# Kernel optimization log

Hardware: AMD Instinct MI355X
Metric: run time of the kernel (lower is better)

Reference implementation:

```python
import jax, jax.numpy as jnp
import numpy as np

N_NODES = 100000
N_EDGES = 1000000

def _gcn_conv(x, W, b, src, dst, n_nodes):
    # PyG GCNConv: linear first, then symmetric-normalized aggregation with self loops
    x = x @ W  # [N, F_out]
    loop = jnp.arange(n_nodes, dtype=src.dtype)
    src2 = jnp.concatenate([src, loop])
    dst2 = jnp.concatenate([dst, loop])
    deg = jax.ops.segment_sum(jnp.ones(src2.shape[0], x.dtype), dst2, num_segments=n_nodes)
    dinv = jnp.where(deg > 0, jax.lax.rsqrt(deg), 0.0)
    norm = dinv[src2] * dinv[dst2]  # [E+N]
    msgs = x[src2] * norm[:, None]  # gather + scale
    out = jax.ops.segment_sum(msgs, dst2, num_segments=n_nodes)  # scatter-add
    return out + b

def _pair_norm_si(x):
    # mode 'PN-SI', scale=1
    x = x - x.mean(axis=0)
    row_norm = jnp.sqrt(1e-6 + jnp.sum(x * x, axis=1, keepdims=True))
    return x / row_norm

def setup_inputs() -> dict:
    key = jax.random.key(0)
    k1, k2, k3, k4 = jax.random.split(key, 4)
    in_c, hid_c, out_c = 256, 64, 40
    x = jax.random.normal(k1, (N_NODES, in_c), dtype=jnp.float32)
    edge_index = jax.random.randint(k2, (2, N_EDGES), 0, N_NODES, dtype=jnp.int64)
    W1 = jax.random.normal(k3, (in_c, hid_c), dtype=jnp.float32) / np.sqrt(in_c)
    b1 = jnp.zeros((hid_c,), jnp.float32)
    W2 = jax.random.normal(k4, (hid_c, out_c), dtype=jnp.float32) / np.sqrt(hid_c)
    b2 = jnp.zeros((out_c,), jnp.float32)
    return {"x": x, "edge_index": edge_index, "W1": W1, "b1": b1, "W2": W2, "b2": b2}

def reference(x, edge_index, W1, b1, W2, b2):
    src, dst = edge_index[0], edge_index[1]
    n = x.shape[0]
    h = jax.nn.relu(_gcn_conv(x, W1, b1, src, dst, n))
    h = _gcn_conv(h, W2, b2, src, dst, n)
    h = _pair_norm_si(h)
    return jax.nn.log_softmax(h, axis=1)
```

## Files before the change

### kernel.cpp

```cpp
#include <hip/hip_runtime.h>
#include <hip/hip_fp16.h>
#include <math.h>

#define F_IN  256
#define F_HID 64
#define F_OUT 40
#define HS2_LD 64

typedef _Float16 h8 __attribute__((ext_vector_type(8)));
typedef _Float16 h4 __attribute__((ext_vector_type(4)));
typedef float f4 __attribute__((ext_vector_type(4)));

__global__ void k_deg(const int* __restrict__ dst, unsigned* __restrict__ degc, int E) {
    int i = blockIdx.x * blockDim.x + threadIdx.x;
    if (i < E) atomicAdd(&degc[dst[i]], 1u);
}

__global__ __launch_bounds__(256) void k_scanA(const unsigned* __restrict__ degc,
                                               unsigned* __restrict__ exscan,
                                               unsigned* __restrict__ bsum, int N) {
    __shared__ unsigned s[256];
    int tid = threadIdx.x;
    int i = blockIdx.x * 256 + tid;
    unsigned v = (i < N) ? ((degc[i] + 8u) & ~7u) : 0u;
    s[tid] = v;
    __syncthreads();
    for (int off = 1; off < 256; off <<= 1) {
        unsigned t = (tid >= off) ? s[tid - off] : 0u;
        __syncthreads();
        s[tid] += t;
        __syncthreads();
    }
    if (i < N) exscan[i] = s[tid] - v;
    if (tid == 255) bsum[blockIdx.x] = s[255];
}

__global__ __launch_bounds__(512) void k_scanB(unsigned* __restrict__ bsum, int nb) {
    __shared__ unsigned s[512];
    int tid = threadIdx.x;
    unsigned v = (tid < nb) ? bsum[tid] : 0u;
    s[tid] = v;
    __syncthreads();
    for (int off = 1; off < 512; off <<= 1) {
        unsigned t = (tid >= off) ? s[tid - off] : 0u;
        __syncthreads();
        s[tid] += t;
        __syncthreads();
    }
    if (tid < nb) bsum[tid] = s[tid] - v;
}

__global__ void k_scanC(const unsigned* __restrict__ degc, const unsigned* __restrict__ exscan,
                        const unsigned* __restrict__ bsum, unsigned* __restrict__ rowptr,
                        float* __restrict__ dinv, int N) {
    int i = blockIdx.x * blockDim.x + threadIdx.x;
    if (i < N) {
        unsigned rp = exscan[i] + bsum[i >> 8];
        rowptr[i] = rp;
        dinv[i] = rsqrtf((float)degc[i] + 1.0f);
        if (i == N - 1) rowptr[N] = rp + ((degc[i] + 8u) & ~7u);
        if (i == 0) dinv[N] = 1.0f;
    }
}

__global__ void k_fill(const int* __restrict__ src, const int* __restrict__ dst,
                       const unsigned* __restrict__ rowptr, unsigned* __restrict__ cursor,
                       unsigned* __restrict__ colp, int E) {
    int e = blockIdx.x * blockDim.x + threadIdx.x;
    if (e >= E) return;
    int d = dst[e];
    unsigned p = atomicAdd(&cursor[d], 1u);
    colp[rowptr[d] + p] = (unsigned)src[e];
}

__global__ void k_pad(const unsigned* __restrict__ degc, const unsigned* __restrict__ rowptr,
                      unsigned* __restrict__ colp, int N) {
    int i = blockIdx.x * blockDim.x + threadIdx.x;
    if (i >= N) return;
    unsigned d = degc[i];
    unsigned base = rowptr[i];
    unsigned pd = (d + 8u) & ~7u;
    colp[base + d] = (unsigned)i;
    for (unsigned p = d + 1; p < pd; ++p) colp[base + p] = (unsigned)N;
}

__global__ void k_wt(const float* __restrict__ W1, __half* __restrict__ Wt) {
    int i = blockIdx.x * 256 + threadIdx.x;
    int k = i >> 6, n = i & 63;
    Wt[n * 256 + k] = __float2half(W1[i]);
}

__global__ void k_w2t(const float* __restrict__ W2, __half* __restrict__ W2t) {
    int i = blockIdx.x * 256 + threadIdx.x;
    int n = i >> 6, k = i & 63;
    W2t[n * 64 + k] = __float2half((n < F_OUT) ? W2[k * F_OUT + n] : 0.f);
}

#define XS 136
__global__ __launch_bounds__(256) void k_mm1(const float* __restrict__ x,
                                             const __half* __restrict__ Wth,
                                             const float* __restrict__ dinv,
                                             __half* __restrict__ hs1o, int N) {
    __shared__ _Float16 sX[64 * XS];
    const _Float16* Wt = (const _Float16*)Wth;
    _Float16* hs1 = (_Float16*)hs1o;
    int tid = threadIdx.x;
    int lane = tid & 63;
    int wv = tid >> 6;
    int m15 = lane & 15;
    int q = lane >> 4;
    int nbase = blockIdx.x * 64;

    h8 bf[8];
    #pragma unroll
    for (int kt = 0; kt < 8; ++kt)
        bf[kt] = *(const h8*)(Wt + (wv * 16 + m15) * 256 + kt * 32 + q * 8);

    f4 acc[4];
    #pragma unroll
    for (int mt = 0; mt < 4; ++mt) acc[mt] = (f4){0.f, 0.f, 0.f, 0.f};

    #pragma unroll
    for (int c = 0; c < 2; ++c) {
        #pragma unroll
        for (int p = 0; p < 8; ++p) {
            int idx = p * 256 + tid;
            int row = idx >> 5;
            int c4  = idx & 31;
            int node = nbase + row;
            float4 v = (node < N) ? *(const float4*)(x + (size_t)node * F_IN + c * 128 + c4 * 4)
                                  : make_float4(0.f, 0.f, 0.f, 0.f);
            h4 hv = { (_Float16)v.x, (_Float16)v.y, (_Float16)v.z, (_Float16)v.w };
            *(h4*)&sX[row * XS + c4 * 4] = hv;
        }
        __syncthreads();
        #pragma unroll
        for (int kt2 = 0; kt2 < 4; ++kt2) {
            #pragma unroll
            for (int mt = 0; mt < 4; ++mt) {
                h8 a = *(const h8*)&sX[(mt * 16 + m15) * XS + kt2 * 32 + q * 8];
                acc[mt] = __builtin_amdgcn_mfma_f32_16x16x32_f16(a, bf[c * 4 + kt2], acc[mt], 0, 0, 0);
            }
        }
        __syncthreads();
    }

    #pragma unroll
    for (int mt = 0; mt < 4; ++mt) {
        #pragma unroll
        for (int r = 0; r < 4; ++r) {
            int node = nbase + mt * 16 + q * 4 + r;
            if (node <= N) {
                float din = (node < N) ? dinv[node] : 1.0f;
                hs1[(size_t)node * F_HID + wv * 16 + m15] = (_Float16)(acc[mt][r] * din);
            }
        }
    }
}

__global__ __launch_bounds__(256) void k_agg1(const unsigned* __restrict__ rowptr,
                                              const unsigned* __restrict__ colp,
                                              const float* __restrict__ dinv,
                                              const __half* __restrict__ hs1o,
                                              const float* __restrict__ bias1,
                                              __half* __restrict__ agg1o, int N) {
    const _Float16* hp = (const _Float16*)hs1o;
    _Float16* agg1h = (_Float16*)agg1o;
    int lane = threadIdx.x & 63;
    int w = blockIdx.x * 4 + (threadIdx.x >> 6);
    int na = 2 * w, nb = 2 * w + 1;
    if (na >= N) return;
    int g = lane >> 3, c = lane & 7;

    float accA[8], accB[8];
    #pragma unroll
    for (int j = 0; j < 8; ++j) { accA[j] = 0.f; accB[j] = 0.f; }

    unsigned aE = rowptr[na], aEnd = rowptr[na + 1];
    bool hasB = (nb < N);
    unsigned bE = 0, bEnd = 0;
    if (hasB) { bE = rowptr[nb]; bEnd = rowptr[nb + 1]; }

    while (aE < aEnd && bE < bEnd) {
        unsigned sA = colp[aE + g];
        unsigned sB = colp[bE + g];
        h8 va = *(const h8*)(hp + (size_t)sA * F_HID + c * 8);
        h8 vb = *(const h8*)(hp + (size_t)sB * F_HID + c * 8);
        #pragma unroll
        for (int j = 0; j < 8; ++j) { accA[j] += (float)va[j]; accB[j] += (float)vb[j]; }
        aE += 8; bE += 8;
    }
    while (aE < aEnd) {
        unsigned sA = colp[aE + g];
        h8 va = *(const h8*)(hp + (size_t)sA * F_HID + c * 8);
        #pragma unroll
        for (int j = 0; j < 8; ++j) accA[j] += (float)va[j];
        aE += 8;
    }
    while (bE < bEnd) {
        unsigned sB = colp[bE + g];
        h8 vb = *(const h8*)(hp + (size_t)sB * F_HID + c * 8);
        #pragma unroll
        for (int j = 0; j < 8; ++j) accB[j] += (float)vb[j];
        bE += 8;
    }

    #pragma unroll
    for (int off = 8; off <= 32; off <<= 1) {
        #pragma unroll
        for (int j = 0; j < 8; ++j) {
            accA[j] += __shfl_xor(accA[j], off, 64);
            accB[j] += __shfl_xor(accB[j], off, 64);
        }
    }

    if (g == 0) {
        float bv[8];
        *(float4*)&bv[0] = *(const float4*)(bias1 + c * 8);
        *(float4*)&bv[4] = *(const float4*)(bias1 + c * 8 + 4);
        float dinA = dinv[na];
        h8 ho;
        #pragma unroll
        for (int j = 0; j < 8; ++j) ho[j] = (_Float16)fmaxf(accA[j] * dinA + bv[j], 0.f);
        *(h8*)(agg1h + (size_t)na * F_HID + c * 8) = ho;
        if (hasB) {
            float dinB = dinv[nb];
            #pragma unroll
            for (int j = 0; j < 8; ++j) ho[j] = (_Float16)fmaxf(accB[j] * dinB + bv[j], 0.f);
            *(h8*)(agg1h + (size_t)nb * F_HID + c * 8) = ho;
        }
    }
}

#define AS 72
__global__ __launch_bounds__(256) void k_mm2(const __half* __restrict__ agg1o,
                                             const __half* __restrict__ W2th,
                                             const float* __restrict__ dinv,
                                             __half* __restrict__ hs2o, int N) {
    __shared__ _Float16 sA[64 * AS];
    const _Float16* agg1h = (const _Float16*)agg1o;
    const _Float16* W2t = (const _Float16*)W2th;
    _Float16* hs2 = (_Float16*)hs2o;
    int tid = threadIdx.x;
    int lane = tid & 63;
    int wv = tid >> 6;
    int m15 = lane & 15;
    int q = lane >> 4;
    int nbase = blockIdx.x * 64;

    h8 bf[2];
    #pragma unroll
    for (int kt = 0; kt < 2; ++kt)
        bf[kt] = *(const h8*)(W2t + (wv * 16 + m15) * 64 + kt * 32 + q * 8);

    #pragma unroll
    for (int p = 0; p < 2; ++p) {
        int idx = p * 256 + tid;
        int row = idx >> 3;
        int c8  = idx & 7;
        int node = nbase + row;
        h8 v;
        if (node < N) v = *(const h8*)(agg1h + (size_t)node * F_HID + c8 * 8);
        else          v = (h8){0, 0, 0, 0, 0, 0, 0, 0};
        *(h8*)&sA[row * AS + c8 * 8] = v;
    }
    __syncthreads();

    f4 acc[4];
    #pragma unroll
    for (int mt = 0; mt < 4; ++mt) acc[mt] = (f4){0.f, 0.f, 0.f, 0.f};
    #pragma unroll
    for (int kt = 0; kt < 2; ++kt) {
        #pragma unroll
        for (int mt = 0; mt < 4; ++mt) {
            h8 a = *(const h8*)&sA[(mt * 16 + m15) * AS + kt * 32 + q * 8];
            acc[mt] = __builtin_amdgcn_mfma_f32_16x16x32_f16(a, bf[kt], acc[mt], 0, 0, 0);
        }
    }

    #pragma unroll
    for (int mt = 0; mt < 4; ++mt) {
        #pragma unroll
        for (int r = 0; r < 4; ++r) {
            int node = nbase + mt * 16 + q * 4 + r;
            if (node <= N) {
                float din = (node < N) ? dinv[node] : 1.0f;
                hs2[(size_t)node * HS2_LD + wv * 16 + m15] = (_Float16)(acc[mt][r] * din);
            }
        }
    }
}

__global__ __launch_bounds__(256) void k_agg2(const unsigned* __restrict__ rowptr,
                                              const unsigned* __restrict__ colp,
                                              const float* __restrict__ dinv,
                                              const __half* __restrict__ hs2o,
                                              float* __restrict__ out,
                                              float* __restrict__ colsum, int N) {
    __shared__ float part[4][8][8];
    const _Float16* hp = (const _Float16*)hs2o;
    int lane = threadIdx.x & 63;
    int wv = threadIdx.x >> 6;
    int g = lane >> 3, c = lane & 7;
    int nwaves = gridDim.x * 4;
    float csum[8];
    #pragma unroll
    for (int j = 0; j < 8; ++j) csum[j] = 0.f;

    for (int w = blockIdx.x * 4 + wv; 2 * w < N; w += nwaves) {
        int na = 2 * w, nb = 2 * w + 1;
        float accA[8], accB[8];
        #pragma unroll
        for (int j = 0; j < 8; ++j) { accA[j] = 0.f; accB[j] = 0.f; }

        unsigned aE = rowptr[na], aEnd = rowptr[na + 1];
        bool hasB = (nb < N);
        unsigned bE = 0, bEnd = 0;
        if (hasB) { bE = rowptr[nb]; bEnd = rowptr[nb + 1]; }

        while (aE < aEnd && bE < bEnd) {
            unsigned sA = colp[aE + g];
            unsigned sB = colp[bE + g];
            h8 va = *(const h8*)(hp + (size_t)sA * HS2_LD + c * 8);
            h8 vb = *(const h8*)(hp + (size_t)sB * HS2_LD + c * 8);
            #pragma unroll
            for (int j = 0; j < 8; ++j) { accA[j] += (float)va[j]; accB[j] += (float)vb[j]; }
            aE += 8; bE += 8;
        }
        while (aE < aEnd) {
            unsigned sA = colp[aE + g];
            h8 va = *(const h8*)(hp + (size_t)sA * HS2_LD + c * 8);
            #pragma unroll
            for (int j = 0; j < 8; ++j) accA[j] += (float)va[j];
            aE += 8;
        }
        while (bE < bEnd) {
            unsigned sB = colp[bE + g];
            h8 vb = *(const h8*)(hp + (size_t)sB * HS2_LD + c * 8);
            #pragma unroll
            for (int j = 0; j < 8; ++j) accB[j] += (float)vb[j];
            bE += 8;
        }

        #pragma unroll
        for (int off = 8; off <= 32; off <<= 1) {
            #pragma unroll
            for (int j = 0; j < 8; ++j) {
                accA[j] += __shfl_xor(accA[j], off, 64);
                accB[j] += __shfl_xor(accB[j], off, 64);
            }
        }

        if (g == 0) {
            float dinA = dinv[na];
            #pragma unroll
            for (int j = 0; j < 8; ++j) { accA[j] *= dinA; csum[j] += accA[j]; }
            if (c < 5) {
                *(float4*)(out + (size_t)na * F_OUT + c * 8) =
                    make_float4(accA[0], accA[1], accA[2], accA[3]);
                *(float4*)(out + (size_t)na * F_OUT + c * 8 + 4) =
                    make_float4(accA[4], accA[5], accA[6], accA[7]);
            }
            if (hasB) {
                float dinB = dinv[nb];
                #pragma unroll
                for (int j = 0; j < 8; ++j) { accB[j] *= dinB; csum[j] += accB[j]; }
                if (c < 5) {
                    *(float4*)(out + (size_t)nb * F_OUT + c * 8) =
                        make_float4(accB[0], accB[1], accB[2], accB[3]);
                    *(float4*)(out + (size_t)nb * F_OUT + c * 8 + 4) =
                        make_float4(accB[4], accB[5], accB[6], accB[7]);
                }
            }
        }
    }

    if (g == 0) {
        #pragma unroll
        for (int j = 0; j < 8; ++j) part[wv][c][j] = csum[j];
    }
    __syncthreads();
    int tid = threadIdx.x;
    if (tid < F_OUT) {
        int cc = tid >> 3, jj = tid & 7;
        float s = part[0][cc][jj] + part[1][cc][jj] + part[2][cc][jj] + part[3][cc][jj];
        atomicAdd(&colsum[tid], s);
    }
}

__global__ __launch_bounds__(128) void k_final(float* __restrict__ out,
                                               const float* __restrict__ colsum, int N) {
    __shared__ float sMean[F_OUT];
    if (threadIdx.x < F_OUT) sMean[threadIdx.x] = colsum[threadIdx.x] * (1.0f / (float)N);
    __syncthreads();
    int n = blockIdx.x * blockDim.x + threadIdx.x;
    if (n >= N) return;
    float* row = out + (size_t)n * F_OUT;
    float v[F_OUT];
    float ss = 0.f;
    #pragma unroll
    for (int f = 0; f < F_OUT; ++f) {
        float t = row[f] - sMean[f];
        v[f] = t;
        ss += t * t;
    }
    float scale = 1.0f / sqrtf(ss + 1e-6f);
    float m = -1e30f;
    #pragma unroll
    for (int f = 0; f < F_OUT; ++f) {
        float y = v[f] * scale;
        v[f] = y;
        m = fmaxf(m, y);
    }
    float sum = 0.f;
    #pragma unroll
    for (int f = 0; f < F_OUT; ++f) sum += expf(v[f] - m);
    float lse = logf(sum);
    #pragma unroll
    for (int f = 0; f < F_OUT; ++f) row[f] = v[f] - m - lse;
}

extern "C" void kernel_launch(void* const* d_in, const int* in_sizes, int n_in,
                              void* d_out, int out_size, void* d_ws, size_t ws_size,
                              hipStream_t stream) {
    const float* x  = (const float*)d_in[0];
    const int*   ei = (const int*)d_in[1];
    const float* W1 = (const float*)d_in[2];
    const float* b1 = (const float*)d_in[3];
    const float* W2 = (const float*)d_in[4];
    float* out = (float*)d_out;

    int N = in_sizes[0] / F_IN;
    int E = in_sizes[1] / 2;
    const int* src = ei;
    const int* dst = ei + E;

    char* p = (char*)d_ws;
    auto alloc = [&](size_t bytes) { char* r = p; p += (bytes + 127) & ~(size_t)127; return r; };
    unsigned* degc   = (unsigned*)alloc((size_t)N * 4);
    unsigned* cursor = (unsigned*)alloc((size_t)N * 4);
    float*    colsum = (float*)   alloc(64 * 4);
    unsigned* rowptr = (unsigned*)alloc((size_t)(N + 1) * 4);
    unsigned* colp   = (unsigned*)alloc((size_t)(E + 8 * N + 8) * 4);
    float*    dinv   = (float*)   alloc((size_t)(N + 1) * 4);
    __half*   agg1h  = (__half*)  alloc((size_t)64 * (N + 1) * 2);
    __half*   hs1    = (__half*)  alloc((size_t)64 * (N + 1) * 2);
    __half*   hs2    = (__half*)  alloc((size_t)64 * (N + 1) * 2);
    __half*   Wt     = (__half*)  alloc((size_t)16384 * 2);
    __half*   W2t    = (__half*)  alloc((size_t)4096 * 2);
    unsigned* exscan = (unsigned*)agg1h;
    unsigned* bsum   = exscan + N;

    hipMemsetAsync(d_ws, 0, (char*)(colsum + 64) - (char*)d_ws, stream);

    int nA = (N + 255) / 256;
    k_deg<<<(E + 255) / 256, 256, 0, stream>>>(dst, degc, E);
    k_scanA<<<nA, 256, 0, stream>>>(degc, exscan, bsum, N);
    k_scanB<<<1, 512, 0, stream>>>(bsum, nA);
    k_scanC<<<nA, 256, 0, stream>>>(degc, exscan, bsum, rowptr, dinv, N);
    k_fill<<<(E + 255) / 256, 256, 0, stream>>>(src, dst, rowptr, cursor, colp, E);
    k_pad<<<nA, 256, 0, stream>>>(degc, rowptr, colp, N);
    k_wt<<<64, 256, 0, stream>>>(W1, Wt);
    k_w2t<<<16, 256, 0, stream>>>(W2, W2t);
    k_mm1<<<(N + 63) / 64, 256, 0, stream>>>(x, Wt, dinv, hs1, N);
    int waves1 = (N + 1) / 2;
    k_agg1<<<(waves1 + 3) / 4, 256, 0, stream>>>(rowptr, colp, dinv, hs1, b1, agg1h, N);
    k_mm2<<<(N + 64) / 64, 256, 0, stream>>>(agg1h, W2t, dinv, hs2, N);
    k_agg2<<<2048, 256, 0, stream>>>(rowptr, colp, dinv, hs2, out, colsum, N);
    k_final<<<(N + 127) / 128, 128, 0, stream>>>(out, colsum, N);
}
```

Measured before the change: 404.8 us.

## Store layer-2 features in FP8 and merge fill/pad and weight-prep launches

Layer-2 pre-aggregation features are written as FP8 e4m3 bytes instead of fp16, which halves the bytes gathered per edge in the second aggregation kernel. The fill and pad kernels are merged into one launch, and the two weight-transpose kernels become a single launch, cutting launch overhead. The FP8 storage lowers precision of the intermediate features and adds per-element decode work in the gather loop, which may affect accuracy tolerance.

```diff
diff --git a/kernel.cpp b/kernel.cpp
--- a/kernel.cpp
+++ b/kernel.cpp
@@ -1,15 +1,20 @@
 #include <hip/hip_runtime.h>
 #include <hip/hip_fp16.h>
+#include <hip/hip_fp8.h>
 #include <math.h>
 
 #define F_IN  256
 #define F_HID 64
 #define F_OUT 40
-#define HS2_LD 64
+#define HS2B  64
 
 typedef _Float16 h8 __attribute__((ext_vector_type(8)));
 typedef _Float16 h4 __attribute__((ext_vector_type(4)));
 typedef float f4 __attribute__((ext_vector_type(4)));
+
+__device__ inline float f8tof(unsigned b) {
+    __hip_fp8_e4m3 t; t.__x = (__hip_fp8_storage_t)b; return (float)t;
+}
 
 __global__ void k_deg(const int* __restrict__ dst, unsigned* __restrict__ degc, int E) {
     int i = blockIdx.x * blockDim.x + threadIdx.x;
@@ -63,37 +68,36 @@
     }
 }
 
-__global__ void k_fill(const int* __restrict__ src, const int* __restrict__ dst,
-                       const unsigned* __restrict__ rowptr, unsigned* __restrict__ cursor,
-                       unsigned* __restrict__ colp, int E) {
-    int e = blockIdx.x * blockDim.x + threadIdx.x;
-    if (e >= E) return;
-    int d = dst[e];
-    unsigned p = atomicAdd(&cursor[d], 1u);
-    colp[rowptr[d] + p] = (unsigned)src[e];
-}
-
-__global__ void k_pad(const unsigned* __restrict__ degc, const unsigned* __restrict__ rowptr,
-                      unsigned* __restrict__ colp, int N) {
-    int i = blockIdx.x * blockDim.x + threadIdx.x;
-    if (i >= N) return;
-    unsigned d = degc[i];
-    unsigned base = rowptr[i];
-    unsigned pd = (d + 8u) & ~7u;
-    colp[base + d] = (unsigned)i;
-    for (unsigned p = d + 1; p < pd; ++p) colp[base + p] = (unsigned)N;
-}
-
-__global__ void k_wt(const float* __restrict__ W1, __half* __restrict__ Wt) {
+__global__ void k_fillpad(const int* __restrict__ src, const int* __restrict__ dst,
+                          const unsigned* __restrict__ degc,
+                          const unsigned* __restrict__ rowptr, unsigned* __restrict__ cursor,
+                          unsigned* __restrict__ colp, int E, int N) {
+    int t = blockIdx.x * blockDim.x + threadIdx.x;
+    if (t < E) {
+        int d = dst[t];
+        unsigned p = atomicAdd(&cursor[d], 1u);
+        colp[rowptr[d] + p] = (unsigned)src[t];
+    } else if (t < E + N) {
+        int i = t - E;
+        unsigned d = degc[i];
+        unsigned base = rowptr[i];
+        unsigned pd = (d + 8u) & ~7u;
+        colp[base + d] = (unsigned)i;
+        for (unsigned p = d + 1; p < pd; ++p) colp[base + p] = (unsigned)N;
+    }
+}
+
+__global__ void k_wprep(const float* __restrict__ W1, const float* __restrict__ W2,
+                        __half* __restrict__ Wt, __half* __restrict__ W2t) {
     int i = blockIdx.x * 256 + threadIdx.x;
-    int k = i >> 6, n = i & 63;
-    Wt[n * 256 + k] = __float2half(W1[i]);
-}
-
-__global__ void k_w2t(const float* __restrict__ W2, __half* __restrict__ W2t) {
-    int i = blockIdx.x * 256 + threadIdx.x;
-    int n = i >> 6, k = i & 63;
-    W2t[n * 64 + k] = __float2half((n < F_OUT) ? W2[k * F_OUT + n] : 0.f);
+    if (i < 16384) {
+        int k = i >> 6, n = i & 63;
+        Wt[n * 256 + k] = __float2half(W1[i]);
+    } else if (i < 20480) {
+        int j = i - 16384;
+        int n = j >> 6, k = j & 63;
+        W2t[n * 64 + k] = __float2half((n < F_OUT) ? W2[k * F_OUT + n] : 0.f);
+    }
 }
 
 #define XS 136
@@ -236,11 +240,10 @@
 __global__ __launch_bounds__(256) void k_mm2(const __half* __restrict__ agg1o,
                                              const __half* __restrict__ W2th,
                                              const float* __restrict__ dinv,
-                                             __half* __restrict__ hs2o, int N) {
+                                             unsigned char* __restrict__ hs2b, int N) {
     __shared__ _Float16 sA[64 * AS];
     const _Float16* agg1h = (const _Float16*)agg1o;
     const _Float16* W2t = (const _Float16*)W2th;
-    _Float16* hs2 = (_Float16*)hs2o;
     int tid = threadIdx.x;
     int lane = tid & 63;
     int wv = tid >> 6;
@@ -285,7 +288,8 @@
             int node = nbase + mt * 16 + q * 4 + r;
             if (node <= N) {
                 float din = (node < N) ? dinv[node] : 1.0f;
-                hs2[(size_t)node * HS2_LD + wv * 16 + m15] = (_Float16)(acc[mt][r] * din);
+                __hip_fp8_e4m3 f8((float)(acc[mt][r] * din));
+                hs2b[(size_t)node * HS2B + wv * 16 + m15] = (unsigned char)f8.__x;
             }
         }
     }
@@ -294,11 +298,10 @@
 __global__ __launch_bounds__(256) void k_agg2(const unsigned* __restrict__ rowptr,
                                               const unsigned* __restrict__ colp,
                                               const float* __restrict__ dinv,
-                                              const __half* __restrict__ hs2o,
+                                              const unsigned char* __restrict__ hs2b,
                                               float* __restrict__ out,
                                               float* __restrict__ colsum, int N) {
     __shared__ float part[4][8][8];
-    const _Float16* hp = (const _Float16*)hs2o;
     int lane = threadIdx.x & 63;
     int wv = threadIdx.x >> 6;
     int g = lane >> 3, c = lane & 7;
@@ -321,24 +324,35 @@
         while (aE < aEnd && bE < bEnd) {
             unsigned sA = colp[aE + g];
             unsigned sB = colp[bE + g];
-            h8 va = *(const h8*)(hp + (size_t)sA * HS2_LD + c * 8);
-            h8 vb = *(const h8*)(hp + (size_t)sB * HS2_LD + c * 8);
-            #pragma unroll
-            for (int j = 0; j < 8; ++j) { accA[j] += (float)va[j]; accB[j] += (float)vb[j]; }
+            uint2 va = *(const uint2*)(hs2b + (size_t)sA * HS2B + c * 8);
+            uint2 vb = *(const uint2*)(hs2b + (size_t)sB * HS2B + c * 8);
+            #pragma unroll
+            for (int j = 0; j < 4; ++j) {
+                accA[j]     += f8tof((va.x >> (8 * j)) & 0xFF);
+                accA[j + 4] += f8tof((va.y >> (8 * j)) & 0xFF);
+                accB[j]     += f8tof((vb.x >> (8 * j)) & 0xFF);
+                accB[j + 4] += f8tof((vb.y >> (8 * j)) & 0xFF);
+            }
             aE += 8; bE += 8;
         }
         while (aE < aEnd) {
             unsigned sA = colp[aE + g];
-            h8 va = *(const h8*)(hp + (size_t)sA * HS2_LD + c * 8);
-            #pragma unroll
-            for (int j = 0; j < 8; ++j) accA[j] += (float)va[j];
+            uint2 va = *(const uint2*)(hs2b + (size_t)sA * HS2B + c * 8);
+            #pragma unroll
+            for (int j = 0; j < 4; ++j) {
+                accA[j]     += f8tof((va.x >> (8 * j)) & 0xFF);
+                accA[j + 4] += f8tof((va.y >> (8 * j)) & 0xFF);
+            }
             aE += 8;
         }
         while (bE < bEnd) {
             unsigned sB = colp[bE + g];
-            h8 vb = *(const h8*)(hp + (size_t)sB * HS2_LD + c * 8);
-            #pragma unroll
-            for (int j = 0; j < 8; ++j) accB[j] += (float)vb[j];
+            uint2 vb = *(const uint2*)(hs2b + (size_t)sB * HS2B + c * 8);
+            #pragma unroll
+            for (int j = 0; j < 4; ++j) {
+                accB[j]     += f8tof((vb.x >> (8 * j)) & 0xFF);
+                accB[j + 4] += f8tof((vb.y >> (8 * j)) & 0xFF);
+            }
             bE += 8;
         }
 
@@ -445,7 +459,7 @@
     float*    dinv   = (float*)   alloc((size_t)(N + 1) * 4);
     __half*   agg1h  = (__half*)  alloc((size_t)64 * (N + 1) * 2);
     __half*   hs1    = (__half*)  alloc((size_t)64 * (N + 1) * 2);
-    __half*   hs2    = (__half*)  alloc((size_t)64 * (N + 1) * 2);
+    unsigned char* hs2b = (unsigned char*)alloc((size_t)HS2B * (N + 1));
     __half*   Wt     = (__half*)  alloc((size_t)16384 * 2);
     __half*   W2t    = (__half*)  alloc((size_t)4096 * 2);
     unsigned* exscan = (unsigned*)agg1h;
@@ -458,14 +472,12 @@
     k_scanA<<<nA, 256, 0, stream>>>(degc, exscan, bsum, N);
     k_scanB<<<1, 512, 0, stream>>>(bsum, nA);
     k_scanC<<<nA, 256, 0, stream>>>(degc, exscan, bsum, rowptr, dinv, N);
-    k_fill<<<(E + 255) / 256, 256, 0, stream>>>(src, dst, rowptr, cursor, colp, E);
-    k_pad<<<nA, 256, 0, stream>>>(degc, rowptr, colp, N);
-    k_wt<<<64, 256, 0, stream>>>(W1, Wt);
-    k_w2t<<<16, 256, 0, stream>>>(W2, W2t);
+    k_fillpad<<<(E + N + 255) / 256, 256, 0, stream>>>(src, dst, degc, rowptr, cursor, colp, E, N);
+    k_wprep<<<80, 256, 0, stream>>>(W1, W2, Wt, W2t);
     k_mm1<<<(N + 63) / 64, 256, 0, stream>>>(x, Wt, dinv, hs1, N);
     int waves1 = (N + 1) / 2;
     k_agg1<<<(waves1 + 3) / 4, 256, 0, stream>>>(rowptr, colp, dinv, hs1, b1, agg1h, N);
-    k_mm2<<<(N + 64) / 64, 256, 0, stream>>>(agg1h, W2t, dinv, hs2, N);
-    k_agg2<<<2048, 256, 0, stream>>>(rowptr, colp, dinv, hs2, out, colsum, N);
+    k_mm2<<<(N + 64) / 64, 256, 0, stream>>>(agg1h, W2t, dinv, hs2b, N);
+    k_agg2<<<2048, 256, 0, stream>>>(rowptr, colp, dinv, hs2b, out, colsum, N);
     k_final<<<(N + 127) / 128, 128, 0, stream>>>(out, colsum, N);
 }
```

Measured after the change: 406.4 us. No clear change (+0.4%).

## Fuse layer-1 aggregation into second matmul and merge small setup kernels

Applied to the files above, without the earlier changes.

Combines the first-layer gather/aggregation with the second-layer MFMA matmul, so the aggregated, ReLU'd features go straight into shared memory instead of a global agg1 buffer that gets written and read back. It also merges the CSR fill and pad kernels into one launch, and the two weight-transpose kernels into one. This cuts a global round trip of an N×64 half tensor and three kernel launches. In exchange, each block now runs 8 sequential node-pair aggregation passes per wave, which lowers parallelism per launch and may expose gather latency.

```diff
diff --git a/kernel.cpp b/kernel.cpp
--- a/kernel.cpp
+++ b/kernel.cpp
@@ -63,37 +63,36 @@
     }
 }
 
-__global__ void k_fill(const int* __restrict__ src, const int* __restrict__ dst,
-                       const unsigned* __restrict__ rowptr, unsigned* __restrict__ cursor,
-                       unsigned* __restrict__ colp, int E) {
-    int e = blockIdx.x * blockDim.x + threadIdx.x;
-    if (e >= E) return;
-    int d = dst[e];
-    unsigned p = atomicAdd(&cursor[d], 1u);
-    colp[rowptr[d] + p] = (unsigned)src[e];
-}
-
-__global__ void k_pad(const unsigned* __restrict__ degc, const unsigned* __restrict__ rowptr,
-                      unsigned* __restrict__ colp, int N) {
-    int i = blockIdx.x * blockDim.x + threadIdx.x;
-    if (i >= N) return;
-    unsigned d = degc[i];
-    unsigned base = rowptr[i];
-    unsigned pd = (d + 8u) & ~7u;
-    colp[base + d] = (unsigned)i;
-    for (unsigned p = d + 1; p < pd; ++p) colp[base + p] = (unsigned)N;
-}
-
-__global__ void k_wt(const float* __restrict__ W1, __half* __restrict__ Wt) {
+__global__ void k_fillpad(const int* __restrict__ src, const int* __restrict__ dst,
+                          const unsigned* __restrict__ degc,
+                          const unsigned* __restrict__ rowptr, unsigned* __restrict__ cursor,
+                          unsigned* __restrict__ colp, int E, int N) {
+    int t = blockIdx.x * blockDim.x + threadIdx.x;
+    if (t < E) {
+        int d = dst[t];
+        unsigned p = atomicAdd(&cursor[d], 1u);
+        colp[rowptr[d] + p] = (unsigned)src[t];
+    } else if (t < E + N) {
+        int i = t - E;
+        unsigned d = degc[i];
+        unsigned base = rowptr[i];
+        unsigned pd = (d + 8u) & ~7u;
+        colp[base + d] = (unsigned)i;
+        for (unsigned p = d + 1; p < pd; ++p) colp[base + p] = (unsigned)N;
+    }
+}
+
+__global__ void k_wprep(const float* __restrict__ W1, const float* __restrict__ W2,
+                        __half* __restrict__ Wt, __half* __restrict__ W2t) {
     int i = blockIdx.x * 256 + threadIdx.x;
-    int k = i >> 6, n = i & 63;
-    Wt[n * 256 + k] = __float2half(W1[i]);
-}
-
-__global__ void k_w2t(const float* __restrict__ W2, __half* __restrict__ W2t) {
-    int i = blockIdx.x * 256 + threadIdx.x;
-    int n = i >> 6, k = i & 63;
-    W2t[n * 64 + k] = __float2half((n < F_OUT) ? W2[k * F_OUT + n] : 0.f);
+    if (i < 16384) {
+        int k = i >> 6, n = i & 63;
+        Wt[n * 256 + k] = __float2half(W1[i]);
+    } else if (i < 20480) {
+        int j = i - 16384;
+        int n = j >> 6, k = j & 63;
+        W2t[n * 64 + k] = __float2half((n < F_OUT) ? W2[k * F_OUT + n] : 0.f);
+    }
 }
 
 #define XS 136
@@ -158,87 +157,16 @@
     }
 }
 
-__global__ __launch_bounds__(256) void k_agg1(const unsigned* __restrict__ rowptr,
-                                              const unsigned* __restrict__ colp,
-                                              const float* __restrict__ dinv,
-                                              const __half* __restrict__ hs1o,
-                                              const float* __restrict__ bias1,
-                                              __half* __restrict__ agg1o, int N) {
+#define AS 72
+__global__ __launch_bounds__(256) void k_aggmm2(const unsigned* __restrict__ rowptr,
+                                                const unsigned* __restrict__ colp,
+                                                const float* __restrict__ dinv,
+                                                const __half* __restrict__ hs1o,
+                                                const float* __restrict__ bias1,
+                                                const __half* __restrict__ W2th,
+                                                __half* __restrict__ hs2o, int N) {
+    __shared__ _Float16 sA[64 * AS];
     const _Float16* hp = (const _Float16*)hs1o;
-    _Float16* agg1h = (_Float16*)agg1o;
-    int lane = threadIdx.x & 63;
-    int w = blockIdx.x * 4 + (threadIdx.x >> 6);
-    int na = 2 * w, nb = 2 * w + 1;
-    if (na >= N) return;
-    int g = lane >> 3, c = lane & 7;
-
-    float accA[8], accB[8];
-    #pragma unroll
-    for (int j = 0; j < 8; ++j) { accA[j] = 0.f; accB[j] = 0.f; }
-
-    unsigned aE = rowptr[na], aEnd = rowptr[na + 1];
-    bool hasB = (nb < N);
-    unsigned bE = 0, bEnd = 0;
-    if (hasB) { bE = rowptr[nb]; bEnd = rowptr[nb + 1]; }
-
-    while (aE < aEnd && bE < bEnd) {
-        unsigned sA = colp[aE + g];
-        unsigned sB = colp[bE + g];
-        h8 va = *(const h8*)(hp + (size_t)sA * F_HID + c * 8);
-        h8 vb = *(const h8*)(hp + (size_t)sB * F_HID + c * 8);
-        #pragma unroll
-        for (int j = 0; j < 8; ++j) { accA[j] += (float)va[j]; accB[j] += (float)vb[j]; }
-        aE += 8; bE += 8;
-    }
-    while (aE < aEnd) {
-        unsigned sA = colp[aE + g];
-        h8 va = *(const h8*)(hp + (size_t)sA * F_HID + c * 8);
-        #pragma unroll
-        for (int j = 0; j < 8; ++j) accA[j] += (float)va[j];
-        aE += 8;
-    }
-    while (bE < bEnd) {
-        unsigned sB = colp[bE + g];
-        h8 vb = *(const h8*)(hp + (size_t)sB * F_HID + c * 8);
-        #pragma unroll
-        for (int j = 0; j < 8; ++j) accB[j] += (float)vb[j];
-        bE += 8;
-    }
-
-    #pragma unroll
-    for (int off = 8; off <= 32; off <<= 1) {
-        #pragma unroll
-        for (int j = 0; j < 8; ++j) {
-            accA[j] += __shfl_xor(accA[j], off, 64);
-            accB[j] += __shfl_xor(accB[j], off, 64);
-        }
-    }
-
-    if (g == 0) {
-        float bv[8];
-        *(float4*)&bv[0] = *(const float4*)(bias1 + c * 8);
-        *(float4*)&bv[4] = *(const float4*)(bias1 + c * 8 + 4);
-        float dinA = dinv[na];
-        h8 ho;
-        #pragma unroll
-        for (int j = 0; j < 8; ++j) ho[j] = (_Float16)fmaxf(accA[j] * dinA + bv[j], 0.f);
-        *(h8*)(agg1h + (size_t)na * F_HID + c * 8) = ho;
-        if (hasB) {
-            float dinB = dinv[nb];
-            #pragma unroll
-            for (int j = 0; j < 8; ++j) ho[j] = (_Float16)fmaxf(accB[j] * dinB + bv[j], 0.f);
-            *(h8*)(agg1h + (size_t)nb * F_HID + c * 8) = ho;
-        }
-    }
-}
-
-#define AS 72
-__global__ __launch_bounds__(256) void k_mm2(const __half* __restrict__ agg1o,
-                                             const __half* __restrict__ W2th,
-                                             const float* __restrict__ dinv,
-                                             __half* __restrict__ hs2o, int N) {
-    __shared__ _Float16 sA[64 * AS];
-    const _Float16* agg1h = (const _Float16*)agg1o;
     const _Float16* W2t = (const _Float16*)W2th;
     _Float16* hs2 = (_Float16*)hs2o;
     int tid = threadIdx.x;
@@ -246,23 +174,77 @@
     int wv = tid >> 6;
     int m15 = lane & 15;
     int q = lane >> 4;
+    int g = lane >> 3, c = lane & 7;
     int nbase = blockIdx.x * 64;
 
-    h8 bf[2];
+    h8 bfW[2];
     #pragma unroll
     for (int kt = 0; kt < 2; ++kt)
-        bf[kt] = *(const h8*)(W2t + (wv * 16 + m15) * 64 + kt * 32 + q * 8);
-
-    #pragma unroll
-    for (int p = 0; p < 2; ++p) {
-        int idx = p * 256 + tid;
-        int row = idx >> 3;
-        int c8  = idx & 7;
-        int node = nbase + row;
-        h8 v;
-        if (node < N) v = *(const h8*)(agg1h + (size_t)node * F_HID + c8 * 8);
-        else          v = (h8){0, 0, 0, 0, 0, 0, 0, 0};
-        *(h8*)&sA[row * AS + c8 * 8] = v;
+        bfW[kt] = *(const h8*)(W2t + (wv * 16 + m15) * 64 + kt * 32 + q * 8);
+
+    float bv[8];
+    *(float4*)&bv[0] = *(const float4*)(bias1 + c * 8);
+    *(float4*)&bv[4] = *(const float4*)(bias1 + c * 8 + 4);
+
+    for (int p2 = 0; p2 < 8; ++p2) {
+        int rowA = wv * 16 + 2 * p2;
+        int na = nbase + rowA, nb = na + 1;
+        bool doA = (na < N), doB = (nb < N);
+
+        float accA[8], accB[8];
+        #pragma unroll
+        for (int j = 0; j < 8; ++j) { accA[j] = 0.f; accB[j] = 0.f; }
+
+        unsigned aE = 0, aEnd = 0, bE = 0, bEnd = 0;
+        if (doA) { aE = rowptr[na]; aEnd = rowptr[na + 1]; }
+        if (doB) { bE = rowptr[nb]; bEnd = rowptr[nb + 1]; }
+
+        while (aE < aEnd && bE < bEnd) {
+            unsigned sAi = colp[aE + g];
+            unsigned sBi = colp[bE + g];
+            h8 va = *(const h8*)(hp + (size_t)sAi * F_HID + c * 8);
+            h8 vb = *(const h8*)(hp + (size_t)sBi * F_HID + c * 8);
+            #pragma unroll
+            for (int j = 0; j < 8; ++j) { accA[j] += (float)va[j]; accB[j] += (float)vb[j]; }
+            aE += 8; bE += 8;
+        }
+        while (aE < aEnd) {
+            unsigned sAi = colp[aE + g];
+            h8 va = *(const h8*)(hp + (size_t)sAi * F_HID + c * 8);
+            #pragma unroll
+            for (int j = 0; j < 8; ++j) accA[j] += (float)va[j];
+            aE += 8;
+        }
+        while (bE < bEnd) {
+            unsigned sBi = colp[bE + g];
+            h8 vb = *(const h8*)(hp + (size_t)sBi * F_HID + c * 8);
+            #pragma unroll
+            for (int j = 0; j < 8; ++j) accB[j] += (float)vb[j];
+            bE += 8;
+        }
+
+        #pragma unroll
+        for (int off = 8; off <= 32; off <<= 1) {
+            #pragma unroll
+            for (int j = 0; j < 8; ++j) {
+                accA[j] += __shfl_xor(accA[j], off, 64);
+                accB[j] += __shfl_xor(accB[j], off, 64);
+            }
+        }
+
+        if (g == 0) {
+            h8 ho;
+            float dinA = doA ? dinv[na] : 0.f;
+            #pragma unroll
+            for (int j = 0; j < 8; ++j)
+                ho[j] = doA ? (_Float16)fmaxf(accA[j] * dinA + bv[j], 0.f) : (_Float16)0.f;
+            *(h8*)&sA[rowA * AS + c * 8] = ho;
+            float dinB = doB ? dinv[nb] : 0.f;
+            #pragma unroll
+            for (int j = 0; j < 8; ++j)
+                ho[j] = doB ? (_Float16)fmaxf(accB[j] * dinB + bv[j], 0.f) : (_Float16)0.f;
+            *(h8*)&sA[(rowA + 1) * AS + c * 8] = ho;
+        }
     }
     __syncthreads();
 
@@ -274,7 +256,7 @@
         #pragma unroll
         for (int mt = 0; mt < 4; ++mt) {
             h8 a = *(const h8*)&sA[(mt * 16 + m15) * AS + kt * 32 + q * 8];
-            acc[mt] = __builtin_amdgcn_mfma_f32_16x16x32_f16(a, bf[kt], acc[mt], 0, 0, 0);
+            acc[mt] = __builtin_amdgcn_mfma_f32_16x16x32_f16(a, bfW[kt], acc[mt], 0, 0, 0);
         }
     }
 
@@ -443,12 +425,11 @@
     unsigned* rowptr = (unsigned*)alloc((size_t)(N + 1) * 4);
     unsigned* colp   = (unsigned*)alloc((size_t)(E + 8 * N + 8) * 4);
     float*    dinv   = (float*)   alloc((size_t)(N + 1) * 4);
-    __half*   agg1h  = (__half*)  alloc((size_t)64 * (N + 1) * 2);
     __half*   hs1    = (__half*)  alloc((size_t)64 * (N + 1) * 2);
     __half*   hs2    = (__half*)  alloc((size_t)64 * (N + 1) * 2);
     __half*   Wt     = (__half*)  alloc((size_t)16384 * 2);
     __half*   W2t    = (__half*)  alloc((size_t)4096 * 2);
-    unsigned* exscan = (unsigned*)agg1h;
+    unsigned* exscan = (unsigned*)hs2;
     unsigned* bsum   = exscan + N;
 
     hipMemsetAsync(d_ws, 0, (char*)(colsum + 64) - (char*)d_ws, stream);
@@ -458,14 +439,10 @@
     k_scanA<<<nA, 256, 0, stream>>>(degc, exscan, bsum, N);
     k_scanB<<<1, 512, 0, stream>>>(bsum, nA);
     k_scanC<<<nA, 256, 0, stream>>>(degc, exscan, bsum, rowptr, dinv, N);
-    k_fill<<<(E + 255) / 256, 256, 0, stream>>>(src, dst, rowptr, cursor, colp, E);
-    k_pad<<<nA, 256, 0, stream>>>(degc, rowptr, colp, N);
-    k_wt<<<64, 256, 0, stream>>>(W1, Wt);
-    k_w2t<<<16, 256, 0, stream>>>(W2, W2t);
+    k_fillpad<<<(E + N + 255) / 256, 256, 0, stream>>>(src, dst, degc, rowptr, cursor, colp, E, N);
+    k_wprep<<<80, 256, 0, stream>>>(W1, W2, Wt, W2t);
     k_mm1<<<(N + 63) / 64, 256, 0, stream>>>(x, Wt, dinv, hs1, N);
-    int waves1 = (N + 1) / 2;
-    k_agg1<<<(waves1 + 3) / 4, 256, 0, stream>>>(rowptr, colp, dinv, hs1, b1, agg1h, N);
-    k_mm2<<<(N + 64) / 64, 256, 0, stream>>>(agg1h, W2t, dinv, hs2, N);
+    k_aggmm2<<<(N + 64) / 64, 256, 0, stream>>>(rowptr, colp, dinv, hs1, b1, W2t, hs2, N);
     k_agg2<<<2048, 256, 0, stream>>>(rowptr, colp, dinv, hs2, out, colsum, N);
     k_final<<<(N + 127) / 128, 128, 0, stream>>>(out, colsum, N);
 }
```

Measured after the change: 416.0 us. +2.8%, slower.

## Fuse CSR-build preprocessing kernels and use single-pass decoupled-lookback scan

Applied to the files above, without the earlier changes.

Merges degree counting with the weight transposes, replaces the three-kernel scan with one decoupled-lookback scan that also zeroes cursor and colsum, and merges edge fill with row padding. This cuts the preprocessing from eight launches to three and shrinks the memset, reducing launch gaps and small-kernel tails. The lookback spins on flag words, so it depends on blocks taking tickets in order and on forward progress. Padding now uses eight threads per node.

```diff
diff --git a/kernel.cpp b/kernel.cpp
--- a/kernel.cpp
+++ b/kernel.cpp
@@ -11,18 +11,42 @@
 typedef _Float16 h4 __attribute__((ext_vector_type(4)));
 typedef float f4 __attribute__((ext_vector_type(4)));
 
-__global__ void k_deg(const int* __restrict__ dst, unsigned* __restrict__ degc, int E) {
-    int i = blockIdx.x * blockDim.x + threadIdx.x;
-    if (i < E) atomicAdd(&degc[dst[i]], 1u);
-}
-
-__global__ __launch_bounds__(256) void k_scanA(const unsigned* __restrict__ degc,
-                                               unsigned* __restrict__ exscan,
-                                               unsigned* __restrict__ bsum, int N) {
+__global__ void k_degw(const int* __restrict__ dst, unsigned* __restrict__ degc, int E,
+                       const float* __restrict__ W1, const float* __restrict__ W2,
+                       __half* __restrict__ Wt, __half* __restrict__ W2t) {
+    int i = blockIdx.x * 256 + threadIdx.x;
+    if (i < E) {
+        atomicAdd(&degc[dst[i]], 1u);
+        return;
+    }
+    int j = i - E;
+    if (j < 16384) {
+        int k = j >> 6, n = j & 63;
+        Wt[n * 256 + k] = __float2half(W1[j]);
+    } else if (j < 20480) {
+        int jj = j - 16384;
+        int n = jj >> 6, k = jj & 63;
+        W2t[n * 64 + k] = __float2half((n < F_OUT) ? W2[k * F_OUT + n] : 0.f);
+    }
+}
+
+__global__ __launch_bounds__(256) void k_scan(const unsigned* __restrict__ degc,
+                                              unsigned* __restrict__ aggf,
+                                              unsigned* __restrict__ ticket,
+                                              unsigned* __restrict__ rowptr,
+                                              float* __restrict__ dinv,
+                                              unsigned* __restrict__ cursor,
+                                              float* __restrict__ colsum, int N) {
     __shared__ unsigned s[256];
+    __shared__ unsigned sTick, sPfx, sTot;
     int tid = threadIdx.x;
-    int i = blockIdx.x * 256 + tid;
-    unsigned v = (i < N) ? ((degc[i] + 8u) & ~7u) : 0u;
+    if (tid == 0) sTick = atomicAdd(ticket, 1u);
+    if (blockIdx.x == 0 && tid < 64) colsum[tid] = 0.f;
+    __syncthreads();
+    unsigned b = sTick;
+    int i = (int)b * 256 + tid;
+    unsigned d = (i < N) ? degc[i] : 0u;
+    unsigned v = (i < N) ? ((d + 8u) & ~7u) : 0u;
     s[tid] = v;
     __syncthreads();
     for (int off = 1; off < 256; off <<= 1) {
@@ -31,69 +55,55 @@
         s[tid] += t;
         __syncthreads();
     }
-    if (i < N) exscan[i] = s[tid] - v;
-    if (tid == 255) bsum[blockIdx.x] = s[255];
-}
-
-__global__ __launch_bounds__(512) void k_scanB(unsigned* __restrict__ bsum, int nb) {
-    __shared__ unsigned s[512];
-    int tid = threadIdx.x;
-    unsigned v = (tid < nb) ? bsum[tid] : 0u;
-    s[tid] = v;
-    __syncthreads();
-    for (int off = 1; off < 512; off <<= 1) {
-        unsigned t = (tid >= off) ? s[tid - off] : 0u;
-        __syncthreads();
-        s[tid] += t;
-        __syncthreads();
-    }
-    if (tid < nb) bsum[tid] = s[tid] - v;
-}
-
-__global__ void k_scanC(const unsigned* __restrict__ degc, const unsigned* __restrict__ exscan,
-                        const unsigned* __restrict__ bsum, unsigned* __restrict__ rowptr,
-                        float* __restrict__ dinv, int N) {
-    int i = blockIdx.x * blockDim.x + threadIdx.x;
+    unsigned incl = s[tid];
+    if (tid == 255) {
+        sTot = s[255];
+        atomicExch(&aggf[b], s[255] | 0x40000000u);
+    }
+    __syncthreads();
+    if (tid == 0) {
+        unsigned run = 0;
+        int pr = (int)b - 1;
+        while (pr >= 0) {
+            unsigned t;
+            do { t = atomicAdd(&aggf[pr], 0u); } while ((t >> 30) == 0u);
+            run += t & 0x3FFFFFFFu;
+            if ((t >> 30) == 3u) break;
+            --pr;
+        }
+        sPfx = run;
+        atomicExch(&aggf[b], (run + sTot) | 0xC0000000u);
+    }
+    __syncthreads();
+    unsigned pfx = sPfx;
     if (i < N) {
-        unsigned rp = exscan[i] + bsum[i >> 8];
-        rowptr[i] = rp;
-        dinv[i] = rsqrtf((float)degc[i] + 1.0f);
-        if (i == N - 1) rowptr[N] = rp + ((degc[i] + 8u) & ~7u);
-        if (i == 0) dinv[N] = 1.0f;
-    }
-}
-
-__global__ void k_fill(const int* __restrict__ src, const int* __restrict__ dst,
-                       const unsigned* __restrict__ rowptr, unsigned* __restrict__ cursor,
-                       unsigned* __restrict__ colp, int E) {
-    int e = blockIdx.x * blockDim.x + threadIdx.x;
-    if (e >= E) return;
-    int d = dst[e];
-    unsigned p = atomicAdd(&cursor[d], 1u);
-    colp[rowptr[d] + p] = (unsigned)src[e];
-}
-
-__global__ void k_pad(const unsigned* __restrict__ degc, const unsigned* __restrict__ rowptr,
-                      unsigned* __restrict__ colp, int N) {
-    int i = blockIdx.x * blockDim.x + threadIdx.x;
-    if (i >= N) return;
-    unsigned d = degc[i];
-    unsigned base = rowptr[i];
-    unsigned pd = (d + 8u) & ~7u;
-    colp[base + d] = (unsigned)i;
-    for (unsigned p = d + 1; p < pd; ++p) colp[base + p] = (unsigned)N;
-}
-
-__global__ void k_wt(const float* __restrict__ W1, __half* __restrict__ Wt) {
-    int i = blockIdx.x * 256 + threadIdx.x;
-    int k = i >> 6, n = i & 63;
-    Wt[n * 256 + k] = __float2half(W1[i]);
-}
-
-__global__ void k_w2t(const float* __restrict__ W2, __half* __restrict__ W2t) {
-    int i = blockIdx.x * 256 + threadIdx.x;
-    int n = i >> 6, k = i & 63;
-    W2t[n * 64 + k] = __float2half((n < F_OUT) ? W2[k * F_OUT + n] : 0.f);
+        rowptr[i] = pfx + incl - v;
+        dinv[i] = rsqrtf((float)d + 1.0f);
+        cursor[i] = 0u;
+        if (i == N - 1) rowptr[N] = pfx + incl;
+    }
+    if (i == 0) dinv[N] = 1.0f;
+}
+
+__global__ void k_fillpad(const int* __restrict__ src, const int* __restrict__ dst,
+                          const unsigned* __restrict__ degc,
+                          const unsigned* __restrict__ rowptr, unsigned* __restrict__ cursor,
+                          unsigned* __restrict__ colp, int E, int N) {
+    int t = blockIdx.x * blockDim.x + threadIdx.x;
+    if (t < E) {
+        int d = dst[t];
+        unsigned p = atomicAdd(&cursor[d], 1u);
+        colp[rowptr[d] + p] = (unsigned)src[t];
+    } else {
+        int r = t - E;
+        int i = r >> 3, j = r & 7;
+        if (i < N) {
+            unsigned d = degc[i];
+            unsigned pd = (d + 8u) & ~7u;
+            unsigned slot = d + (unsigned)j;
+            if (slot < pd) colp[rowptr[i] + slot] = (j == 0) ? (unsigned)i : (unsigned)N;
+        }
+    }
 }
 
 #define XS 136
@@ -438,6 +448,9 @@
     char* p = (char*)d_ws;
     auto alloc = [&](size_t bytes) { char* r = p; p += (bytes + 127) & ~(size_t)127; return r; };
     unsigned* degc   = (unsigned*)alloc((size_t)N * 4);
+    unsigned* aggf   = (unsigned*)alloc(512 * 4);
+    unsigned* ticket = (unsigned*)alloc(4);
+    char* zend = p;
     unsigned* cursor = (unsigned*)alloc((size_t)N * 4);
     float*    colsum = (float*)   alloc(64 * 4);
     unsigned* rowptr = (unsigned*)alloc((size_t)(N + 1) * 4);
@@ -448,20 +461,13 @@
     __half*   hs2    = (__half*)  alloc((size_t)64 * (N + 1) * 2);
     __half*   Wt     = (__half*)  alloc((size_t)16384 * 2);
     __half*   W2t    = (__half*)  alloc((size_t)4096 * 2);
-    unsigned* exscan = (unsigned*)agg1h;
-    unsigned* bsum   = exscan + N;
-
-    hipMemsetAsync(d_ws, 0, (char*)(colsum + 64) - (char*)d_ws, stream);
+
+    hipMemsetAsync(d_ws, 0, (size_t)(zend - (char*)d_ws), stream);
 
     int nA = (N + 255) / 256;
-    k_deg<<<(E + 255) / 256, 256, 0, stream>>>(dst, degc, E);
-    k_scanA<<<nA, 256, 0, stream>>>(degc, exscan, bsum, N);
-    k_scanB<<<1, 512, 0, stream>>>(bsum, nA);
-    k_scanC<<<nA, 256, 0, stream>>>(degc, exscan, bsum, rowptr, dinv, N);
-    k_fill<<<(E + 255) / 256, 256, 0, stream>>>(src, dst, rowptr, cursor, colp, E);
-    k_pad<<<nA, 256, 0, stream>>>(degc, rowptr, colp, N);
-    k_wt<<<64, 256, 0, stream>>>(W1, Wt);
-    k_w2t<<<16, 256, 0, stream>>>(W2, W2t);
+    k_degw<<<(E + 20480 + 255) / 256, 256, 0, stream>>>(dst, degc, E, W1, W2, Wt, W2t);
+    k_scan<<<nA, 256, 0, stream>>>(degc, aggf, ticket, rowptr, dinv, cursor, colsum, N);
+    k_fillpad<<<(E + 8 * N + 255) / 256, 256, 0, stream>>>(src, dst, degc, rowptr, cursor, colp, E, N);
     k_mm1<<<(N + 63) / 64, 256, 0, stream>>>(x, Wt, dinv, hs1, N);
     int waves1 = (N + 1) / 2;
     k_agg1<<<(waves1 + 3) / 4, 256, 0, stream>>>(rowptr, colp, dinv, hs1, b1, agg1h, N);
```

Result: faster. 396.9 us (-2.0%).
